# Optimization experiments

Hardware: AMD Instinct MI355X
Metric: run time of the kernel (lower is better)

## Reference

```python
import jax, jax.numpy as jnp
import numpy as np

N = 8192
HID = 64
TAU = 0.8
LAMBDA = 0.5
POS_DENSITY = 0.005


def setup_inputs() -> dict:
    key = jax.random.key(0)
    k1, k2, k3, k4, k5, k6, k7 = jax.random.split(key, 7)
    x1 = jax.random.normal(k1, (N, HID), dtype=jnp.float32)
    x2 = jax.random.normal(k2, (N, HID), dtype=jnp.float32)
    # xavier_uniform with gain=1.414 for square [HID, HID] linears
    limit = 1.414 * np.sqrt(6.0 / (HID + HID))
    W1 = jax.random.uniform(k3, (HID, HID), dtype=jnp.float32, minval=-limit, maxval=limit)
    b1 = jnp.zeros((HID,), dtype=jnp.float32)
    W2 = jax.random.uniform(k4, (HID, HID), dtype=jnp.float32, minval=-limit, maxval=limit)
    b2 = jnp.zeros((HID,), dtype=jnp.float32)
    pm = (jax.random.uniform(k5, (N, N), dtype=jnp.float32) < POS_DENSITY).astype(jnp.float32)
    positive_matrix = jnp.maximum(pm, jnp.eye(N, dtype=jnp.float32))
    return {"x1": x1, "x2": x2, "W1": W1, "b1": b1, "W2": W2, "b2": b2,
            "positive_matrix": positive_matrix}


def _project(x, W1, b1, W2, b2):
    # nn.Linear(hidden, hidden) -> ELU -> nn.Linear(hidden, hidden)
    h = jax.nn.elu(x @ W1.T + b1)
    return h @ W2.T + b2


def _l2norm(z, eps=1e-12):
    # F.normalize(p=2, dim=1): x / max(||x||, eps)
    n = jnp.linalg.norm(z, axis=-1, keepdims=True)
    return z / jnp.maximum(n, eps)


def _sim(z1, z2, tau):
    return jnp.exp((_l2norm(z1) @ _l2norm(z2).T) / tau)  # [N, N]


def _masked_loss(sim_mat, pos):
    row = sim_mat / (jnp.sum(sim_mat, axis=-1, keepdims=True) + 1e-8)
    return -jnp.log(jnp.sum(row * pos, axis=-1) + 1e-8).mean()


def reference(x1, x2, W1, b1, W2, b2, positive_matrix):
    z1 = _project(x1, W1, b1, W2, b2)
    z2 = _project(x2, W1, b1, W2, b2)
    sc_mp = _sim(z1, z2, TAU)
    mp_sc = _sim(z2, z1, TAU)
    sc_loss = _masked_loss(sc_mp, positive_matrix)
    mp_loss = _masked_loss(mp_sc, positive_matrix)
    return sc_loss * LAMBDA + mp_loss * (1.0 - LAMBDA)
```

## Files before the change

### kernel.cpp

```cpp
#include <hip/hip_runtime.h>
#include <hip/hip_bf16.h>

#define N 8192
#define HID 64
#define JC 16

typedef __attribute__((ext_vector_type(4))) float f32x4;
typedef __attribute__((ext_vector_type(8))) __bf16 bf16x8;

__global__ __launch_bounds__(256) void proj_kernel(
    const float* __restrict__ x1, const float* __restrict__ x2,
    const float* __restrict__ W1, const float* __restrict__ b1,
    const float* __restrict__ W2, const float* __restrict__ b2,
    __bf16* __restrict__ Z1h, __bf16* __restrict__ Z2h,
    float* __restrict__ stats)
{
  __shared__ __align__(16) float w1s[64*68];
  __shared__ __align__(16) float w2s[64*68];
  __shared__ __align__(16) float xs[4][64];
  __shared__ __align__(16) float hs[4][64];

  const int tid  = threadIdx.x;
  const int lane = tid & 63;
  const int w    = tid >> 6;

  int gtid = blockIdx.x * 256 + tid;
  if (gtid < 4*N) stats[gtid] = 0.f;

  for (int idx = tid; idx < 64*64; idx += 256) {
    int j = idx >> 6, k = idx & 63;
    w1s[j*68+k] = W1[idx];
    w2s[j*68+k] = W2[idx];
  }
  __syncthreads();

  const float bias1 = b1[lane];
  const float bias2 = b2[lane];

  const int wave_global = blockIdx.x * 4 + w;
  #pragma unroll 1
  for (int it = 0; it < 4; ++it) {
    int R = wave_global * 4 + it;
    const float* src; __bf16* dst;
    if (R < N) { src = x1 + (size_t)R*HID;      dst = Z1h + (size_t)R*HID; }
    else       { src = x2 + (size_t)(R-N)*HID;  dst = Z2h + (size_t)(R-N)*HID; }

    float xv = src[lane];
    xs[w][lane] = xv;
    float acc = bias1;
    #pragma unroll
    for (int qq = 0; qq < 16; ++qq) {
      f32x4 xq = *(const f32x4*)&xs[w][qq*4];
      f32x4 wq = *(const f32x4*)&w1s[lane*68 + qq*4];
      acc += xq.x*wq.x + xq.y*wq.y + xq.z*wq.z + xq.w*wq.w;
    }
    float h = acc > 0.f ? acc : expm1f(acc);
    hs[w][lane] = h;
    float acc2 = bias2;
    #pragma unroll
    for (int qq = 0; qq < 16; ++qq) {
      f32x4 hq = *(const f32x4*)&hs[w][qq*4];
      f32x4 wq = *(const f32x4*)&w2s[lane*68 + qq*4];
      acc2 += hq.x*wq.x + hq.y*wq.y + hq.z*wq.z + hq.w*wq.w;
    }
    float z = acc2;
    float ss = z*z;
    #pragma unroll
    for (int m = 1; m < 64; m <<= 1) ss += __shfl_xor(ss, m);
    float inv = 1.0f / fmaxf(sqrtf(ss), 1e-12f);
    dst[lane] = (__bf16)(z * inv);
  }
}

__global__ __launch_bounds__(256) void sim_kernel(
    const __bf16* __restrict__ Z1h, const __bf16* __restrict__ Z2h,
    const float* __restrict__ pos,
    float* __restrict__ rowsum1, float* __restrict__ num1,
    float* __restrict__ rowsum2, float* __restrict__ num2)
{
  const int tid  = threadIdx.x;
  const int lane = tid & 63;
  const int w    = tid >> 6;
  const int r16  = lane & 15;
  const int q    = lane >> 4;

  const int bi = blockIdx.x / JC;
  const int jc = blockIdx.x % JC;
  const int i0 = bi*64 + w*16;

  const __bf16* z1r = Z1h + (size_t)(i0 + r16)*HID + q*8;
  const __bf16* z2r = Z2h + (size_t)(i0 + r16)*HID + q*8;
  const bf16x8 a1lo = *(const bf16x8*)(z1r);
  const bf16x8 a1hi = *(const bf16x8*)(z1r + 32);
  const bf16x8 a2lo = *(const bf16x8*)(z2r);
  const bf16x8 a2hi = *(const bf16x8*)(z2r + 32);

  float s1 = 0.f, n1 = 0.f, s2 = 0.f, n2 = 0.f;

  const int jbeg = jc * (N/JC);
  const float Cexp = 1.8033688011112042f;
  const float* prow = pos + (size_t)(i0 + r16)*N + q*4;

  #pragma unroll 1
  for (int j0 = jbeg; j0 < jbeg + (N/JC); j0 += 32) {
    bf16x8 b2l[2], b2h[2], b1l[2], b1h[2];
    f32x4 pv[2];
    #pragma unroll
    for (int c = 0; c < 2; ++c) {
      const __bf16* zj2 = Z2h + (size_t)(j0 + c*16 + r16)*HID + q*8;
      const __bf16* zj1 = Z1h + (size_t)(j0 + c*16 + r16)*HID + q*8;
      b2l[c] = *(const bf16x8*)(zj2);
      b2h[c] = *(const bf16x8*)(zj2 + 32);
      b1l[c] = *(const bf16x8*)(zj1);
      b1h[c] = *(const bf16x8*)(zj1 + 32);
      pv[c]  = *(const f32x4*)(prow + j0 + c*16);
    }
    #pragma unroll
    for (int c = 0; c < 2; ++c) {
      f32x4 zero4 = {0.f,0.f,0.f,0.f};
      f32x4 d1 = __builtin_amdgcn_mfma_f32_16x16x32_bf16(b2l[c], a1lo, zero4, 0,0,0);
      d1       = __builtin_amdgcn_mfma_f32_16x16x32_bf16(b2h[c], a1hi, d1,    0,0,0);
      f32x4 d2 = __builtin_amdgcn_mfma_f32_16x16x32_bf16(b1l[c], a2lo, zero4, 0,0,0);
      d2       = __builtin_amdgcn_mfma_f32_16x16x32_bf16(b1h[c], a2hi, d2,    0,0,0);
      #pragma unroll
      for (int r = 0; r < 4; ++r) {
        float e1 = exp2f(d1[r] * Cexp);
        float e2 = exp2f(d2[r] * Cexp);
        s1 += e1; n1 += e1 * pv[c][r];
        s2 += e2; n2 += e2 * pv[c][r];
      }
    }
  }

  s1 += __shfl_xor(s1, 16); s1 += __shfl_xor(s1, 32);
  n1 += __shfl_xor(n1, 16); n1 += __shfl_xor(n1, 32);
  s2 += __shfl_xor(s2, 16); s2 += __shfl_xor(s2, 32);
  n2 += __shfl_xor(n2, 16); n2 += __shfl_xor(n2, 32);

  if (lane < 16) {
    int row = i0 + r16;
    atomicAdd(&rowsum1[row], s1);
    atomicAdd(&num1[row],    n1);
    atomicAdd(&rowsum2[row], s2);
    atomicAdd(&num2[row],    n2);
  }
}

__global__ __launch_bounds__(1024) void loss_kernel(
    const float* __restrict__ rowsum1, const float* __restrict__ num1,
    const float* __restrict__ rowsum2, const float* __restrict__ num2,
    float* __restrict__ out)
{
  __shared__ float part[16];
  const int tid = threadIdx.x, lane = tid & 63, w = tid >> 6;
  float acc = 0.f;
  for (int i = tid; i < N; i += 1024) {
    float sc = -logf(num1[i]/(rowsum1[i]+1e-8f) + 1e-8f);
    float mp = -logf(num2[i]/(rowsum2[i]+1e-8f) + 1e-8f);
    acc += 0.5f*sc + 0.5f*mp;
  }
  #pragma unroll
  for (int m = 1; m < 64; m <<= 1) acc += __shfl_xor(acc, m);
  if (lane == 0) part[w] = acc;
  __syncthreads();
  if (tid == 0) {
    float t = 0.f;
    #pragma unroll
    for (int k = 0; k < 16; ++k) t += part[k];
    out[0] = t * (1.0f/N);
  }
}

extern "C" void kernel_launch(void* const* d_in, const int* in_sizes, int n_in,
                              void* d_out, int out_size, void* d_ws, size_t ws_size,
                              hipStream_t stream) {
  const float* x1  = (const float*)d_in[0];
  const float* x2  = (const float*)d_in[1];
  const float* W1  = (const float*)d_in[2];
  const float* b1  = (const float*)d_in[3];
  const float* W2  = (const float*)d_in[4];
  const float* b2  = (const float*)d_in[5];
  const float* pos = (const float*)d_in[6];

  char* ws = (char*)d_ws;
  __bf16* Z1h = (__bf16*)ws;
  __bf16* Z2h = (__bf16*)(ws + (size_t)N*HID*sizeof(__bf16));
  size_t zbytes = (size_t)2*N*HID*sizeof(__bf16);
  float* rowsum1 = (float*)(ws + zbytes);
  float* num1    = rowsum1 + N;
  float* rowsum2 = num1 + N;
  float* num2    = rowsum2 + N;

  proj_kernel<<<1024, 256, 0, stream>>>(x1, x2, W1, b1, W2, b2, Z1h, Z2h, rowsum1);
  sim_kernel<<<128*JC, 256, 0, stream>>>(Z1h, Z2h, pos, rowsum1, num1, rowsum2, num2);
  loss_kernel<<<1, 1024, 0, stream>>>(rowsum1, num1, rowsum2, num2, (float*)d_out);
}
```

Baseline: 462.4 us.

## Double-buffer positive-mask tiles into LDS via async global_load_lds with swizzle

The positive-matrix reads in the similarity kernel are restaged. Each wave asynchronously copies its 16×64 fp32 tile of the mask into a double-buffered LDS region using global_load_lds, with an XOR-swizzled layout, and prefetches the next tile while computing the current one. Per-lane strided 16-byte loads become contiguous 256-byte row segments, and the long-latency mask stream overlaps with the MFMA and exp work. The column split per block is halved (JC 16→8), so there are fewer, longer blocks. That uses 32 KB of LDS per block and relies on hand-written vmcnt waits, which may reduce occupancy.

```diff
diff --git a/kernel.cpp b/kernel.cpp
--- a/kernel.cpp
+++ b/kernel.cpp
@@ -3,10 +3,16 @@
 
 #define N 8192
 #define HID 64
-#define JC 16
+#define JC 8
 
 typedef __attribute__((ext_vector_type(4))) float f32x4;
 typedef __attribute__((ext_vector_type(8))) __bf16 bf16x8;
+
+__device__ __forceinline__ void gload_lds16(const float* g, float* l) {
+  __builtin_amdgcn_global_load_lds(
+      (const __attribute__((address_space(1))) void*)g,
+      (__attribute__((address_space(3))) void*)l, 16, 0, 0);
+}
 
 __global__ __launch_bounds__(256) void proj_kernel(
     const float* __restrict__ x1, const float* __restrict__ x2,
@@ -78,15 +84,18 @@
     float* __restrict__ rowsum1, float* __restrict__ num1,
     float* __restrict__ rowsum2, float* __restrict__ num2)
 {
+  __shared__ __align__(16) float pbuf[2][64][64];
+
   const int tid  = threadIdx.x;
   const int lane = tid & 63;
   const int w    = tid >> 6;
   const int r16  = lane & 15;
   const int q    = lane >> 4;
 
-  const int bi = blockIdx.x / JC;
-  const int jc = blockIdx.x % JC;
-  const int i0 = bi*64 + w*16;
+  const int bi  = blockIdx.x / JC;
+  const int jc  = blockIdx.x % JC;
+  const int i0b = bi*64;
+  const int i0  = i0b + w*16;
 
   const __bf16* z1r = Z1h + (size_t)(i0 + r16)*HID + q*8;
   const __bf16* z2r = Z2h + (size_t)(i0 + r16)*HID + q*8;
@@ -99,38 +108,66 @@
 
   const int jbeg = jc * (N/JC);
   const float Cexp = 1.8033688011112042f;
-  const float* prow = pos + (size_t)(i0 + r16)*N + q*4;
-
+
+#define STAGE(BUF, JJ) { \
+    _Pragma("unroll") \
+    for (int rr = 0; rr < 4; ++rr) { \
+      int row_t = w*16 + rr*4 + (lane >> 4); \
+      int slot  = lane & 15; \
+      const float* gsrc = pos + (size_t)(i0b + row_t)*N + (JJ) + (((slot ^ (row_t & 7))) << 2); \
+      gload_lds16(gsrc, &pbuf[BUF][w*16 + rr*4][0]); \
+    } }
+
+  STAGE(0, jbeg)
+
+  int cur = 0;
   #pragma unroll 1
-  for (int j0 = jbeg; j0 < jbeg + (N/JC); j0 += 32) {
-    bf16x8 b2l[2], b2h[2], b1l[2], b1h[2];
-    f32x4 pv[2];
-    #pragma unroll
-    for (int c = 0; c < 2; ++c) {
-      const __bf16* zj2 = Z2h + (size_t)(j0 + c*16 + r16)*HID + q*8;
-      const __bf16* zj1 = Z1h + (size_t)(j0 + c*16 + r16)*HID + q*8;
-      b2l[c] = *(const bf16x8*)(zj2);
-      b2h[c] = *(const bf16x8*)(zj2 + 32);
-      b1l[c] = *(const bf16x8*)(zj1);
-      b1h[c] = *(const bf16x8*)(zj1 + 32);
-      pv[c]  = *(const f32x4*)(prow + j0 + c*16);
-    }
-    #pragma unroll
-    for (int c = 0; c < 2; ++c) {
-      f32x4 zero4 = {0.f,0.f,0.f,0.f};
-      f32x4 d1 = __builtin_amdgcn_mfma_f32_16x16x32_bf16(b2l[c], a1lo, zero4, 0,0,0);
-      d1       = __builtin_amdgcn_mfma_f32_16x16x32_bf16(b2h[c], a1hi, d1,    0,0,0);
-      f32x4 d2 = __builtin_amdgcn_mfma_f32_16x16x32_bf16(b1l[c], a2lo, zero4, 0,0,0);
-      d2       = __builtin_amdgcn_mfma_f32_16x16x32_bf16(b1h[c], a2hi, d2,    0,0,0);
+  for (int ss = 0; ss < 16; ++ss) {
+    const int jj = jbeg + ss*64;
+    if (ss != 15) {
+      STAGE(cur ^ 1, jj + 64)
+      asm volatile("s_waitcnt vmcnt(4)" ::: "memory");
+    } else {
+      asm volatile("s_waitcnt vmcnt(0)" ::: "memory");
+    }
+    __builtin_amdgcn_sched_barrier(0);
+
+    #pragma unroll
+    for (int cc = 0; cc < 64; cc += 32) {
+      const int j0 = jj + cc;
+      bf16x8 b2l[2], b2h[2], b1l[2], b1h[2];
+      f32x4 pv[2];
       #pragma unroll
-      for (int r = 0; r < 4; ++r) {
-        float e1 = exp2f(d1[r] * Cexp);
-        float e2 = exp2f(d2[r] * Cexp);
-        s1 += e1; n1 += e1 * pv[c][r];
-        s2 += e2; n2 += e2 * pv[c][r];
+      for (int c = 0; c < 2; ++c) {
+        const __bf16* zj2 = Z2h + (size_t)(j0 + c*16 + r16)*HID + q*8;
+        const __bf16* zj1 = Z1h + (size_t)(j0 + c*16 + r16)*HID + q*8;
+        b2l[c] = *(const bf16x8*)(zj2);
+        b2h[c] = *(const bf16x8*)(zj2 + 32);
+        b1l[c] = *(const bf16x8*)(zj1);
+        b1h[c] = *(const bf16x8*)(zj1 + 32);
+        int g = (cc >> 2) + c*4 + q;
+        int s = g ^ (r16 & 7);
+        pv[c] = *(const f32x4*)&pbuf[cur][w*16 + r16][s*4];
       }
-    }
-  }
+      #pragma unroll
+      for (int c = 0; c < 2; ++c) {
+        f32x4 zero4 = {0.f,0.f,0.f,0.f};
+        f32x4 d1 = __builtin_amdgcn_mfma_f32_16x16x32_bf16(b2l[c], a1lo, zero4, 0,0,0);
+        d1       = __builtin_amdgcn_mfma_f32_16x16x32_bf16(b2h[c], a1hi, d1,    0,0,0);
+        f32x4 d2 = __builtin_amdgcn_mfma_f32_16x16x32_bf16(b1l[c], a2lo, zero4, 0,0,0);
+        d2       = __builtin_amdgcn_mfma_f32_16x16x32_bf16(b1h[c], a2hi, d2,    0,0,0);
+        #pragma unroll
+        for (int r = 0; r < 4; ++r) {
+          float e1 = exp2f(d1[r] * Cexp);
+          float e2 = exp2f(d2[r] * Cexp);
+          s1 += e1; n1 += e1 * pv[c][r];
+          s2 += e2; n2 += e2 * pv[c][r];
+        }
+      }
+    }
+    cur ^= 1;
+  }
+#undef STAGE
 
   s1 += __shfl_xor(s1, 16); s1 += __shfl_xor(s1, 32);
   n1 += __shfl_xor(n1, 16); n1 += __shfl_xor(n1, 32);
```

After: 438.2 us. 5.2% less time.

## Double-buffer Z tiles in LDS via global_load_lds and prefetch positive mask

Applied to the files above, without the earlier changes.

The sim kernel now stages 64-row tiles of Z1/Z2 into LDS with direct global-to-LDS loads, using an XOR swizzle to avoid bank conflicts. It double-buffers those tiles and prefetches the matching positive-mask vectors one tile ahead, so global latency overlaps the MFMA and exp work. Because the tiles are shared in LDS, each workgroup no longer has every wave fetch the same column rows separately. JC is halved to 8 so each block runs a longer pipelined loop, and launch bounds request 4 blocks per CU. This adds a barrier per tile and more register pressure from the prefetched mask vectors.

```diff
diff --git a/kernel.cpp b/kernel.cpp
--- a/kernel.cpp
+++ b/kernel.cpp
@@ -3,10 +3,16 @@
 
 #define N 8192
 #define HID 64
-#define JC 16
+#define JC 8
 
 typedef __attribute__((ext_vector_type(4))) float f32x4;
 typedef __attribute__((ext_vector_type(8))) __bf16 bf16x8;
+
+__device__ __forceinline__ void gload_lds16(const void* g, float* l) {
+  __builtin_amdgcn_global_load_lds(
+      (const __attribute__((address_space(1))) void*)g,
+      (__attribute__((address_space(3))) void*)l, 16, 0, 0);
+}
 
 __global__ __launch_bounds__(256) void proj_kernel(
     const float* __restrict__ x1, const float* __restrict__ x2,
@@ -72,21 +78,24 @@
   }
 }
 
-__global__ __launch_bounds__(256) void sim_kernel(
+__global__ __launch_bounds__(256, 4) void sim_kernel(
     const __bf16* __restrict__ Z1h, const __bf16* __restrict__ Z2h,
     const float* __restrict__ pos,
     float* __restrict__ rowsum1, float* __restrict__ num1,
     float* __restrict__ rowsum2, float* __restrict__ num2)
 {
+  __shared__ __align__(16) float zs1[2][2048];
+  __shared__ __align__(16) float zs2[2][2048];
+
   const int tid  = threadIdx.x;
   const int lane = tid & 63;
   const int w    = tid >> 6;
   const int r16  = lane & 15;
   const int q    = lane >> 4;
 
-  const int bi = blockIdx.x / JC;
-  const int jc = blockIdx.x % JC;
-  const int i0 = bi*64 + w*16;
+  const int bi  = blockIdx.x / JC;
+  const int jc  = blockIdx.x % JC;
+  const int i0  = bi*64 + w*16;
 
   const __bf16* z1r = Z1h + (size_t)(i0 + r16)*HID + q*8;
   const __bf16* z2r = Z2h + (size_t)(i0 + r16)*HID + q*8;
@@ -101,36 +110,72 @@
   const float Cexp = 1.8033688011112042f;
   const float* prow = pos + (size_t)(i0 + r16)*N + q*4;
 
+  f32x4 PA0, PA1, PA2, PA3, PB0, PB1, PB2, PB3;
+
+#define STAGEZ(BUF, JJ) { \
+    const int r8 = lane >> 3; \
+    const int sl = (lane & 7) ^ r8; \
+    gload_lds16(Z1h + (size_t)((JJ) + w*16     + r8)*HID + sl*8, &zs1[BUF][(w*16    )*32]); \
+    gload_lds16(Z1h + (size_t)((JJ) + w*16 + 8 + r8)*HID + sl*8, &zs1[BUF][(w*16 + 8)*32]); \
+    gload_lds16(Z2h + (size_t)((JJ) + w*16     + r8)*HID + sl*8, &zs2[BUF][(w*16    )*32]); \
+    gload_lds16(Z2h + (size_t)((JJ) + w*16 + 8 + r8)*HID + sl*8, &zs2[BUF][(w*16 + 8)*32]); \
+  }
+
+#define LOADPOS(P, JJ) { \
+    P##0 = *(const f32x4*)(prow + (JJ)); \
+    P##1 = *(const f32x4*)(prow + (JJ) + 16); \
+    P##2 = *(const f32x4*)(prow + (JJ) + 32); \
+    P##3 = *(const f32x4*)(prow + (JJ) + 48); \
+  }
+
+#define COMPC(BUF, C, CC, PV) { \
+    const int R  = (CC) + (C)*16 + r16; \
+    const int sw = r16 & 7; \
+    bf16x8 b2lo = *(const bf16x8*)&zs2[BUF][R*32 + ((q    ) ^ sw)*4]; \
+    bf16x8 b2hi = *(const bf16x8*)&zs2[BUF][R*32 + ((q + 4) ^ sw)*4]; \
+    bf16x8 b1lo = *(const bf16x8*)&zs1[BUF][R*32 + ((q    ) ^ sw)*4]; \
+    bf16x8 b1hi = *(const bf16x8*)&zs1[BUF][R*32 + ((q + 4) ^ sw)*4]; \
+    f32x4 zero4 = {0.f,0.f,0.f,0.f}; \
+    f32x4 d1 = __builtin_amdgcn_mfma_f32_16x16x32_bf16(b2lo, a1lo, zero4, 0,0,0); \
+    d1       = __builtin_amdgcn_mfma_f32_16x16x32_bf16(b2hi, a1hi, d1,    0,0,0); \
+    f32x4 d2 = __builtin_amdgcn_mfma_f32_16x16x32_bf16(b1lo, a2lo, zero4, 0,0,0); \
+    d2       = __builtin_amdgcn_mfma_f32_16x16x32_bf16(b1hi, a2hi, d2,    0,0,0); \
+    _Pragma("unroll") \
+    for (int r = 0; r < 4; ++r) { \
+      float e1 = exp2f(d1[r] * Cexp); \
+      float e2 = exp2f(d2[r] * Cexp); \
+      s1 += e1; n1 += e1 * PV[r]; \
+      s2 += e2; n2 += e2 * PV[r]; \
+    } }
+
+#define STEP(BUF, P) { COMPC(BUF,0,0,P##0) COMPC(BUF,1,0,P##1) COMPC(BUF,0,32,P##2) COMPC(BUF,1,32,P##3) }
+
+  STAGEZ(0, jbeg)
+  LOADPOS(PA, jbeg)
+  __syncthreads();
+
   #pragma unroll 1
-  for (int j0 = jbeg; j0 < jbeg + (N/JC); j0 += 32) {
-    bf16x8 b2l[2], b2h[2], b1l[2], b1h[2];
-    f32x4 pv[2];
-    #pragma unroll
-    for (int c = 0; c < 2; ++c) {
-      const __bf16* zj2 = Z2h + (size_t)(j0 + c*16 + r16)*HID + q*8;
-      const __bf16* zj1 = Z1h + (size_t)(j0 + c*16 + r16)*HID + q*8;
-      b2l[c] = *(const bf16x8*)(zj2);
-      b2h[c] = *(const bf16x8*)(zj2 + 32);
-      b1l[c] = *(const bf16x8*)(zj1);
-      b1h[c] = *(const bf16x8*)(zj1 + 32);
-      pv[c]  = *(const f32x4*)(prow + j0 + c*16);
-    }
-    #pragma unroll
-    for (int c = 0; c < 2; ++c) {
-      f32x4 zero4 = {0.f,0.f,0.f,0.f};
-      f32x4 d1 = __builtin_amdgcn_mfma_f32_16x16x32_bf16(b2l[c], a1lo, zero4, 0,0,0);
-      d1       = __builtin_amdgcn_mfma_f32_16x16x32_bf16(b2h[c], a1hi, d1,    0,0,0);
-      f32x4 d2 = __builtin_amdgcn_mfma_f32_16x16x32_bf16(b1l[c], a2lo, zero4, 0,0,0);
-      d2       = __builtin_amdgcn_mfma_f32_16x16x32_bf16(b1h[c], a2hi, d2,    0,0,0);
-      #pragma unroll
-      for (int r = 0; r < 4; ++r) {
-        float e1 = exp2f(d1[r] * Cexp);
-        float e2 = exp2f(d2[r] * Cexp);
-        s1 += e1; n1 += e1 * pv[c][r];
-        s2 += e2; n2 += e2 * pv[c][r];
-      }
-    }
-  }
+  for (int tp = 0; tp < 7; ++tp) {
+    const int t0 = tp*2;
+    STAGEZ(1, jbeg + (t0+1)*64)
+    LOADPOS(PB, jbeg + (t0+1)*64)
+    STEP(0, PA)
+    __syncthreads();
+    STAGEZ(0, jbeg + (t0+2)*64)
+    LOADPOS(PA, jbeg + (t0+2)*64)
+    STEP(1, PB)
+    __syncthreads();
+  }
+  STAGEZ(1, jbeg + 15*64)
+  LOADPOS(PB, jbeg + 15*64)
+  STEP(0, PA)
+  __syncthreads();
+  STEP(1, PB)
+
+#undef STAGEZ
+#undef LOADPOS
+#undef COMPC
+#undef STEP
 
   s1 += __shfl_xor(s1, 16); s1 += __shfl_xor(s1, 32);
   n1 += __shfl_xor(n1, 16); n1 += __shfl_xor(n1, 32);
```

Measured after the change: 419.0 us. -9.4%, faster.

## Precompress positive mask to bitmask in coalesced pre-pass, fully unroll sim loop

Applied to the files above, without the earlier changes.

Adds a pre-pass kernel that streams the fp32 positive matrix with fully coalesced reads and packs it into 4-bit-per-float byte masks. The sim kernel then loads that compact mask once up front and uses shuffles to hand each MFMA chunk its bits. This replaces the poorly coalesced strided fp32 loads of the mask inside the hot loop. The sim loop is also fully unrolled. The cost is an extra launch plus a 16MB write and read. It also assumes the mask is binary, since non-zero values are treated as 1.

```diff
diff --git a/kernel.cpp b/kernel.cpp
--- a/kernel.cpp
+++ b/kernel.cpp
@@ -7,6 +7,21 @@
 
 typedef __attribute__((ext_vector_type(4))) float f32x4;
 typedef __attribute__((ext_vector_type(8))) __bf16 bf16x8;
+
+__global__ __launch_bounds__(256) void mask_kernel(
+    const float* __restrict__ pos, unsigned char* __restrict__ mask)
+{
+  int idx = blockIdx.x * 256 + threadIdx.x;
+  const int stride = 2048 * 256;
+  #pragma unroll 1
+  for (int it = 0; it < 32; ++it) {
+    int i = idx + it * stride;
+    f32x4 v = *(const f32x4*)(pos + (size_t)i * 4);
+    unsigned b = (unsigned)(v.x != 0.f) | ((unsigned)(v.y != 0.f) << 1)
+               | ((unsigned)(v.z != 0.f) << 2) | ((unsigned)(v.w != 0.f) << 3);
+    mask[i] = (unsigned char)b;
+  }
+}
 
 __global__ __launch_bounds__(256) void proj_kernel(
     const float* __restrict__ x1, const float* __restrict__ x2,
@@ -74,7 +89,7 @@
 
 __global__ __launch_bounds__(256) void sim_kernel(
     const __bf16* __restrict__ Z1h, const __bf16* __restrict__ Z2h,
-    const float* __restrict__ pos,
+    const unsigned char* __restrict__ mask,
     float* __restrict__ rowsum1, float* __restrict__ num1,
     float* __restrict__ rowsum2, float* __restrict__ num2)
 {
@@ -95,42 +110,63 @@
   const bf16x8 a2lo = *(const bf16x8*)(z2r);
   const bf16x8 a2hi = *(const bf16x8*)(z2r + 32);
 
-  float s1 = 0.f, n1 = 0.f, s2 = 0.f, n2 = 0.f;
-
   const int jbeg = jc * (N/JC);
   const float Cexp = 1.8033688011112042f;
-  const float* prow = pos + (size_t)(i0 + r16)*N + q*4;
-
-  #pragma unroll 1
-  for (int j0 = jbeg; j0 < jbeg + (N/JC); j0 += 32) {
-    bf16x8 b2l[2], b2h[2], b1l[2], b1h[2];
-    f32x4 pv[2];
-    #pragma unroll
-    for (int c = 0; c < 2; ++c) {
-      const __bf16* zj2 = Z2h + (size_t)(j0 + c*16 + r16)*HID + q*8;
-      const __bf16* zj1 = Z1h + (size_t)(j0 + c*16 + r16)*HID + q*8;
-      b2l[c] = *(const bf16x8*)(zj2);
-      b2h[c] = *(const bf16x8*)(zj2 + 32);
-      b1l[c] = *(const bf16x8*)(zj1);
-      b1h[c] = *(const bf16x8*)(zj1 + 32);
-      pv[c]  = *(const f32x4*)(prow + j0 + c*16);
-    }
-    #pragma unroll
-    for (int c = 0; c < 2; ++c) {
-      f32x4 zero4 = {0.f,0.f,0.f,0.f};
-      f32x4 d1 = __builtin_amdgcn_mfma_f32_16x16x32_bf16(b2l[c], a1lo, zero4, 0,0,0);
-      d1       = __builtin_amdgcn_mfma_f32_16x16x32_bf16(b2h[c], a1hi, d1,    0,0,0);
-      f32x4 d2 = __builtin_amdgcn_mfma_f32_16x16x32_bf16(b1l[c], a2lo, zero4, 0,0,0);
-      d2       = __builtin_amdgcn_mfma_f32_16x16x32_bf16(b1h[c], a2hi, d2,    0,0,0);
-      #pragma unroll
-      for (int r = 0; r < 4; ++r) {
-        float e1 = exp2f(d1[r] * Cexp);
-        float e2 = exp2f(d2[r] * Cexp);
-        s1 += e1; n1 += e1 * pv[c][r];
-        s2 += e2; n2 += e2 * pv[c][r];
-      }
-    }
-  }
+
+  const unsigned char* mrow = mask + (size_t)(i0 + r16)*(N/4) + (jbeg >> 2) + q*4;
+  const unsigned MK0 = *(const unsigned*)(mrow + 0*16);
+  const unsigned MK1 = *(const unsigned*)(mrow + 1*16);
+  const unsigned MK2 = *(const unsigned*)(mrow + 2*16);
+  const unsigned MK3 = *(const unsigned*)(mrow + 3*16);
+  const unsigned MK4 = *(const unsigned*)(mrow + 4*16);
+  const unsigned MK5 = *(const unsigned*)(mrow + 5*16);
+  const unsigned MK6 = *(const unsigned*)(mrow + 6*16);
+  const unsigned MK7 = *(const unsigned*)(mrow + 7*16);
+
+  float s1 = 0.f, n1 = 0.f, s2 = 0.f, n2 = 0.f;
+
+#define COMPC(J0, MK) { \
+    const __bf16* zj2 = Z2h + (size_t)((J0) + r16)*HID + q*8; \
+    const __bf16* zj1 = Z1h + (size_t)((J0) + r16)*HID + q*8; \
+    bf16x8 b2lo = *(const bf16x8*)(zj2); \
+    bf16x8 b2hi = *(const bf16x8*)(zj2 + 32); \
+    bf16x8 b1lo = *(const bf16x8*)(zj1); \
+    bf16x8 b1hi = *(const bf16x8*)(zj1 + 32); \
+    f32x4 zero4 = {0.f,0.f,0.f,0.f}; \
+    f32x4 d1 = __builtin_amdgcn_mfma_f32_16x16x32_bf16(b2lo, a1lo, zero4, 0,0,0); \
+    d1       = __builtin_amdgcn_mfma_f32_16x16x32_bf16(b2hi, a1hi, d1,    0,0,0); \
+    f32x4 d2 = __builtin_amdgcn_mfma_f32_16x16x32_bf16(b1lo, a2lo, zero4, 0,0,0); \
+    d2       = __builtin_amdgcn_mfma_f32_16x16x32_bf16(b1hi, a2hi, d2,    0,0,0); \
+    _Pragma("unroll") \
+    for (int r = 0; r < 4; ++r) { \
+      float e1 = exp2f(d1[r] * Cexp); \
+      float e2 = exp2f(d2[r] * Cexp); \
+      s1 += e1; s2 += e2; \
+      if (((MK) >> (8*q + r)) & 1u) { n1 += e1; n2 += e2; } \
+    } }
+
+#define GROUP(G, MKG) { \
+    const int j0 = jbeg + (G)*64; \
+    const unsigned Mk0 = __shfl((int)(MKG),      r16); \
+    const unsigned Mk1 = __shfl((int)(MKG), 16 + r16); \
+    const unsigned Mk2 = __shfl((int)(MKG), 32 + r16); \
+    const unsigned Mk3 = __shfl((int)(MKG), 48 + r16); \
+    COMPC(j0,      Mk0) \
+    COMPC(j0 + 16, Mk1) \
+    COMPC(j0 + 32, Mk2) \
+    COMPC(j0 + 48, Mk3) }
+
+  GROUP(0, MK0)
+  GROUP(1, MK1)
+  GROUP(2, MK2)
+  GROUP(3, MK3)
+  GROUP(4, MK4)
+  GROUP(5, MK5)
+  GROUP(6, MK6)
+  GROUP(7, MK7)
+
+#undef COMPC
+#undef GROUP
 
   s1 += __shfl_xor(s1, 16); s1 += __shfl_xor(s1, 32);
   n1 += __shfl_xor(n1, 16); n1 += __shfl_xor(n1, 32);
@@ -190,8 +226,10 @@
   float* num1    = rowsum1 + N;
   float* rowsum2 = num1 + N;
   float* num2    = rowsum2 + N;
-
+  unsigned char* mask = (unsigned char*)(ws + zbytes + (size_t)4*N*sizeof(float));
+
+  mask_kernel<<<2048, 256, 0, stream>>>(pos, mask);
   proj_kernel<<<1024, 256, 0, stream>>>(x1, x2, W1, b1, W2, b2, Z1h, Z2h, rowsum1);
-  sim_kernel<<<128*JC, 256, 0, stream>>>(Z1h, Z2h, pos, rowsum1, num1, rowsum2, num2);
+  sim_kernel<<<128*JC, 256, 0, stream>>>(Z1h, Z2h, mask, rowsum1, num1, rowsum2, num2);
   loss_kernel<<<1, 1024, 0, stream>>>(rowsum1, num1, rowsum2, num2, (float*)d_out);
 }
```

New measurement: 509.3 us. 1.1x slower.
